# Performance work log

Measured on AMD Instinct MI355X. Metric: run time of the kernel, lower is better.

Reference implementation:

```python
import jax, jax.numpy as jnp
import numpy as np

B, N, IN_DIM, D, H, L = 4, 2048, 1, 256, 8, 4
DH = D // H          # 32 head dim
ROPE_D = DH // 2     # 16 = rotary dim per spatial axis (relative_emb_dim=2)
MIN_FREQ_SCALE = 64.0  # scale / min_freq = 1.0 / (1/64)
EPS = 1e-5


def setup_inputs():
    key = jax.random.key(0)
    ks = jax.random.split(key, 12)
    s = 0.02
    return {
        'h': jax.random.normal(ks[0], (B, N, IN_DIM), jnp.float32),
        'pos': jax.random.uniform(ks[1], (B, N, 2), jnp.float32),
        'proj_w': jax.random.normal(ks[2], (IN_DIM, D), jnp.float32) * s,
        'proj_b': jnp.zeros((D,), jnp.float32),
        'qkv_w': jax.random.normal(ks[3], (L, D, 3 * D), jnp.float32) * s,
        'out_w': jax.random.normal(ks[4], (L, D, D), jnp.float32) * s,
        'out_b': jnp.zeros((L, D), jnp.float32),
        'O_w': jax.random.normal(ks[5], (L, D, D), jnp.float32) * s,
        'O_b': jnp.zeros((L, D), jnp.float32),
        'ffn1_w': jax.random.normal(ks[6], (L, D, 2 * D), jnp.float32) * s,
        'ffn1_b': jnp.zeros((L, 2 * D), jnp.float32),
        'ffn2_w': jax.random.normal(ks[7], (L, 2 * D, D), jnp.float32) * s,
        'ffn2_b': jnp.zeros((L, D), jnp.float32),
        'ln1_g': jnp.ones((L, D), jnp.float32),
        'ln1_b': jnp.zeros((L, D), jnp.float32),
        'ln2_g': jnp.ones((L, D), jnp.float32),
        'ln2_b': jnp.zeros((L, D), jnp.float32),
        'final_w': jax.random.normal(ks[8], (D, D), jnp.float32) * s,
    }


def _rope_freqs(coords):
    # coords: (B, N) -> freqs (B, N, ROPE_D)
    inv_freq = 1.0 / (10000.0 ** (jnp.arange(0, ROPE_D, 2, dtype=jnp.float32) / ROPE_D))
    f = (coords * MIN_FREQ_SCALE)[..., None] * inv_freq
    return jnp.concatenate([f, f], axis=-1)


def _rotate_half(x):
    d = x.shape[-1] // 2
    return jnp.concatenate([-x[..., d:], x[..., :d]], axis=-1)


def _apply_rope(t, f):
    return t * jnp.cos(f) + _rotate_half(t) * jnp.sin(f)


def _apply_2d_rope(t, ft, fx):
    d = t.shape[-1] // 2
    return jnp.concatenate([_apply_rope(t[..., :d], ft), _apply_rope(t[..., d:], fx)], axis=-1)


def _ln(x, g, b):
    m = jnp.mean(x, -1, keepdims=True)
    v = jnp.mean((x - m) ** 2, -1, keepdims=True)
    return (x - m) / jnp.sqrt(v + EPS) * g + b


def _forward(h, pos, proj_w, proj_b, qkv_w, out_w, out_b, O_w, O_b,
             ffn1_w, ffn1_b, ffn2_w, ffn2_b, ln1_g, ln1_b, ln2_g, ln2_b, final_w):
    h = h @ proj_w + proj_b                      # (B, N, D)
    ft = _rope_freqs(pos[..., 0])[:, None]       # (B, 1, N, ROPE_D) broadcast over heads
    fx = _rope_freqs(pos[..., 1])[:, None]
    scale = DH ** -0.5
    for l in range(L):
        qkv = h @ qkv_w[l]                       # (B, N, 3D)
        q, k, v = jnp.split(qkv, 3, axis=-1)
        to_heads = lambda t: t.reshape(B, N, H, DH).transpose(0, 2, 1, 3)
        q, k, v = to_heads(q), to_heads(k), to_heads(v)
        q = _apply_2d_rope(q, ft, fx)
        k = _apply_2d_rope(k, ft, fx)
        attn = jax.nn.softmax(jnp.einsum('bhid,bhjd->bhij', q, k) * scale, axis=-1)
        o = jnp.einsum('bhij,bhjd->bhid', attn, v)
        o = o.transpose(0, 2, 1, 3).reshape(B, N, D)
        o = o @ out_w[l] + out_b[l]              # attention to_out
        o = o @ O_w[l] + O_b[l]                  # layer O projection
        h = _ln(h + o, ln1_g[l], ln1_b[l])
        f = jax.nn.relu(h @ ffn1_w[l] + ffn1_b[l]) @ ffn2_w[l] + ffn2_b[l]
        h = _ln(h + f, ln2_g[l], ln2_b[l])
    return h @ final_w


def reference(h, pos, proj_w, proj_b, qkv_w, out_w, out_b, O_w, O_b,
              ffn1_w, ffn1_b, ffn2_w, ffn2_b, ln1_g, ln1_b, ln2_g, ln2_b, final_w):
    return _forward(h, pos, proj_w, proj_b, qkv_w, out_w, out_b, O_w, O_b,
                    ffn1_w, ffn1_b, ffn2_w, ffn2_b, ln1_g, ln1_b, ln2_g, ln2_b, final_w)
```

## Files before the change

### kernel.cpp

```cpp
#include <hip/hip_runtime.h>
#include <math.h>

#define B_ 4
#define N_ 2048
#define D_ 256
#define H_ 8
#define L_ 4
#define DH_ 32

typedef float f32x4 __attribute__((ext_vector_type(4)));
typedef short short8 __attribute__((ext_vector_type(8)));
typedef unsigned short ushort_t;
typedef ushort_t ushortx4 __attribute__((ext_vector_type(4)));
typedef ushort_t ushortx8 __attribute__((ext_vector_type(8)));

static __device__ __forceinline__ ushort_t f2bf(float x) {
    unsigned int u = __float_as_uint(x);
    unsigned int r = (u + 0x7fffu + ((u >> 16) & 1u)) >> 16;
    return (ushort_t)r;
}

static __device__ __forceinline__ unsigned int cvt_pk_bf16(float a, float b) {
    unsigned int w;
    asm("v_cvt_pk_bf16_f32 %0, %1, %2" : "=v"(w) : "v"(a), "v"(b));
    return w;
}

__global__ __launch_bounds__(256) void proj_kernel(
    const float* __restrict__ hin, const float* __restrict__ w,
    const float* __restrict__ bias, float* __restrict__ hout,
    ushort_t* __restrict__ hb)
{
    long idx = (long)blockIdx.x * 256 + threadIdx.x;
    long bn = idx >> 6;
    int d4 = (int)(idx & 63) << 2;
    float hv = hin[bn];
    float4 wv = *(const float4*)&w[d4];
    float4 bv = *(const float4*)&bias[d4];
    float4 o;
    o.x = hv * wv.x + bv.x;
    o.y = hv * wv.y + bv.y;
    o.z = hv * wv.z + bv.z;
    o.w = hv * wv.w + bv.w;
    *(float4*)&hout[bn * D_ + d4] = o;
    ushortx4 ob;
    ob[0] = f2bf(o.x); ob[1] = f2bf(o.y); ob[2] = f2bf(o.z); ob[3] = f2bf(o.w);
    *(ushortx4*)&hb[bn * D_ + d4] = ob;
}

__global__ __launch_bounds__(256) void rope_table_kernel(
    const float* __restrict__ pos, float* __restrict__ tab)
{
    int i = blockIdx.x * 256 + threadIdx.x;
    if (i >= B_ * N_) return;
    float t = pos[i * 2 + 0] * 64.0f;
    float x = pos[i * 2 + 1] * 64.0f;
    float* o = tab + (long)i * 32;
    const float log2_1e4_over8 = 13.28771237954945f / 8.0f;
    #pragma unroll
    for (int j = 0; j < 8; ++j) {
        float invf = exp2f(-(float)j * log2_1e4_over8);
        float st, ct, sx, cx;
        sincosf(t * invf, &st, &ct);
        sincosf(x * invf, &sx, &cx);
        o[j]      = ct;
        o[8 + j]  = st;
        o[16 + j] = cx;
        o[24 + j] = sx;
    }
}

__global__ __launch_bounds__(256) void rope_convert_kernel(
    const float* __restrict__ qkv, const float* __restrict__ tab,
    ushort_t* __restrict__ Qb, ushort_t* __restrict__ Kb)
{
    const float F = 0.17677669529663687f * 1.4426950408889634f;
    long idx = (long)blockIdx.x * 256 + threadIdx.x;
    int p = (int)(idx & 15);
    int h = (int)((idx >> 4) & 7);
    long bn = idx >> 7;
    int half = p >> 3;
    int j = p & 7;
    const float* tb = tab + bn * 32;
    float c = tb[half * 16 + j];
    float s = tb[half * 16 + 8 + j];
    float cF = c * F, sF = s * F;
    int b = (int)(bn >> 11);
    int n = (int)(bn & 2047);
    long obase = ((long)(b * H_ + h) * N_ + n) * DH_;
    const float* base = qkv + bn * (3 * D_) + h * DH_ + half * 16 + j;
    int d0 = half * 16 + j;
    float q0 = base[0], q1 = base[8];
    Qb[obase + d0]     = f2bf(q0 * cF - q1 * sF);
    Qb[obase + d0 + 8] = f2bf(q1 * cF + q0 * sF);
    float k0 = base[D_], k1 = base[D_ + 8];
    Kb[obase + d0]     = f2bf(k0 * c - k1 * s);
    Kb[obase + d0 + 8] = f2bf(k1 * c + k0 * s);
}

__global__ __launch_bounds__(256) void vtrans_kernel(
    const float* __restrict__ qkv, ushort_t* __restrict__ Vt)
{
    int bh = blockIdx.y;
    int b = bh >> 3, h = bh & 7;
    int n0 = blockIdx.x << 6;
    __shared__ float T[64][36];
    int t = threadIdx.x;
    int r = t >> 2, c0 = (t & 3) << 3;
    const float* src = qkv + ((long)b * N_ + n0 + r) * (3 * D_) + 2 * D_ + h * DH_ + c0;
    float4 a = ((const float4*)src)[0];
    float4 bb = ((const float4*)src)[1];
    *(float4*)&T[r][c0] = a;
    *(float4*)&T[r][c0 + 4] = bb;
    __syncthreads();
    int d = t >> 3, n8 = (t & 7) << 3;
    ushortx8 o;
    #pragma unroll
    for (int i = 0; i < 8; ++i) o[i] = f2bf(T[n8 + i][d]);
    *(ushortx8*)&Vt[((long)bh * DH_ + d) * N_ + n0 + n8] = o;
}

__global__ __launch_bounds__(256) void wprep_kernel(
    const float* __restrict__ qkv_w, const float* __restrict__ out_w,
    const float* __restrict__ O_w, const float* __restrict__ ffn1_w,
    const float* __restrict__ ffn2_w, const float* __restrict__ final_w,
    ushort_t* __restrict__ WT)
{
    int bid = blockIdx.x;
    const float* src; ushort_t* dst; int K, Nn, tile;
    if (bid < 192)      { int l = bid / 48;        tile = bid % 48;        src = qkv_w  + (long)l * 196608; dst = WT + (long)l * 196608;           K = 256; Nn = 768; }
    else if (bid < 256) { int r = bid - 192; int l = r / 16; tile = r % 16; src = out_w  + (long)l * 65536;  dst = WT + 786432  + (long)l * 65536;  K = 256; Nn = 256; }
    else if (bid < 320) { int r = bid - 256; int l = r / 16; tile = r % 16; src = O_w    + (long)l * 65536;  dst = WT + 1048576 + (long)l * 65536;  K = 256; Nn = 256; }
    else if (bid < 448) { int r = bid - 320; int l = r / 32; tile = r % 32; src = ffn1_w + (long)l * 131072; dst = WT + 1310720 + (long)l * 131072; K = 256; Nn = 512; }
    else if (bid < 576) { int r = bid - 448; int l = r / 32; tile = r % 32; src = ffn2_w + (long)l * 131072; dst = WT + 1835008 + (long)l * 131072; K = 512; Nn = 256; }
    else                { tile = bid - 576;                                 src = final_w;                   dst = WT + 2359296;                    K = 256; Nn = 256; }
    int ntn = Nn >> 6;
    int kt = (tile / ntn) << 6;
    int nt = (tile % ntn) << 6;
    __shared__ float Tl[64][65];
    int t = threadIdx.x;
    int kr = t >> 2, nc0 = (t & 3) << 4;
    const float* sp = src + (long)(kt + kr) * Nn + nt + nc0;
    float4 v0 = ((const float4*)sp)[0];
    float4 v1 = ((const float4*)sp)[1];
    float4 v2 = ((const float4*)sp)[2];
    float4 v3 = ((const float4*)sp)[3];
    float* tr = &Tl[kr][nc0];
    tr[0] = v0.x; tr[1] = v0.y; tr[2] = v0.z; tr[3] = v0.w;
    tr[4] = v1.x; tr[5] = v1.y; tr[6] = v1.z; tr[7] = v1.w;
    tr[8] = v2.x; tr[9] = v2.y; tr[10] = v2.z; tr[11] = v2.w;
    tr[12] = v3.x; tr[13] = v3.y; tr[14] = v3.z; tr[15] = v3.w;
    __syncthreads();
    int n = t >> 2, kc0 = (t & 3) << 4;
    ushortx8 o0, o1;
    #pragma unroll
    for (int i = 0; i < 8; ++i) o0[i] = f2bf(Tl[kc0 + i][n]);
    #pragma unroll
    for (int i = 0; i < 8; ++i) o1[i] = f2bf(Tl[kc0 + 8 + i][n]);
    ushort_t* dp = dst + (long)(nt + n) * K + kt + kc0;
    *(ushortx8*)dp = o0;
    *(ushortx8*)(dp + 8) = o1;
}

__global__ __launch_bounds__(256) void gemm_mfma(
    const ushort_t* __restrict__ A, const ushort_t* __restrict__ BT,
    const float* __restrict__ bias, void* __restrict__ Cout,
    int N, int K, int flags)
{
    __shared__ ushort_t sA[64 * 64];
    __shared__ ushort_t sB[64 * 64];
    int tid = threadIdx.x;
    int wid = tid >> 6, lane = tid & 63;
    int lo = lane & 15, hi = lane >> 4;
    int wm = wid >> 1, wn = wid & 1;
    int m0 = blockIdx.y << 6, n0 = blockIdx.x << 6;

    int srow = tid >> 3;
    int sslot = tid & 7;
    const ushort_t* Ap  = A  + (long)(m0 + srow) * K + sslot * 8;
    const ushort_t* Ap2 = Ap + 32 * (long)K;
    const ushort_t* Bp  = BT + (long)(n0 + srow) * K + sslot * 8;
    const ushort_t* Bp2 = Bp + 32 * (long)K;
    int wa1 = srow * 64 + (sslot ^ (srow & 7)) * 8;
    int wa2 = (srow + 32) * 64 + (sslot ^ (srow & 7)) * 8;

    f32x4 acc[2][2];
    #pragma unroll
    for (int i = 0; i < 2; ++i)
        #pragma unroll
        for (int j = 0; j < 2; ++j) acc[i][j] = (f32x4){0.f, 0.f, 0.f, 0.f};

    int ar0 = (wm * 32 + lo) * 64;
    int ar1 = (wm * 32 + 16 + lo) * 64;
    int br0 = (wn * 32 + lo) * 64;
    int br1 = (wn * 32 + 16 + lo) * 64;
    int swz = lo & 7;

    for (int kt = 0; kt < K; kt += 64) {
        ushortx8 a1 = *(const ushortx8*)(Ap + kt);
        ushortx8 a2 = *(const ushortx8*)(Ap2 + kt);
        ushortx8 b1 = *(const ushortx8*)(Bp + kt);
        ushortx8 b2 = *(const ushortx8*)(Bp2 + kt);
        __syncthreads();
        *(ushortx8*)&sA[wa1] = a1;
        *(ushortx8*)&sA[wa2] = a2;
        *(ushortx8*)&sB[wa1] = b1;
        *(ushortx8*)&sB[wa2] = b2;
        __syncthreads();
        #pragma unroll
        for (int kf = 0; kf < 2; ++kf) {
            int ks = ((kf * 4 + hi) ^ swz) * 8;
            short8 a0 = *(const short8*)&sA[ar0 + ks];
            short8 a1f = *(const short8*)&sA[ar1 + ks];
            short8 b0 = *(const short8*)&sB[br0 + ks];
            short8 b1f = *(const short8*)&sB[br1 + ks];
            acc[0][0] = __builtin_amdgcn_mfma_f32_16x16x32_bf16(a0, b0, acc[0][0], 0, 0, 0);
            acc[0][1] = __builtin_amdgcn_mfma_f32_16x16x32_bf16(a0, b1f, acc[0][1], 0, 0, 0);
            acc[1][0] = __builtin_amdgcn_mfma_f32_16x16x32_bf16(a1f, b0, acc[1][0], 0, 0, 0);
            acc[1][1] = __builtin_amdgcn_mfma_f32_16x16x32_bf16(a1f, b1f, acc[1][1], 0, 0, 0);
        }
    }

    #pragma unroll
    for (int nf = 0; nf < 2; ++nf) {
        int col = n0 + wn * 32 + nf * 16 + lo;
        float bv = (flags & 1) ? bias[col] : 0.f;
        #pragma unroll
        for (int mf = 0; mf < 2; ++mf) {
            #pragma unroll
            for (int j = 0; j < 4; ++j) {
                float v = acc[mf][nf][j] + bv;
                if (flags & 2) v = fmaxf(v, 0.f);
                long row = m0 + wm * 32 + mf * 16 + hi * 4 + j;
                if (flags & 4) ((ushort_t*)Cout)[row * N + col] = f2bf(v);
                else           ((float*)Cout)[row * N + col] = v;
            }
        }
    }
}

__global__ __launch_bounds__(256) void attn_mfma2(
    const ushort_t* __restrict__ Qb, const ushort_t* __restrict__ Kb,
    const ushort_t* __restrict__ Vt, ushort_t* __restrict__ o)
{
    int bh = blockIdx.y;
    int tid = threadIdx.x;
    int wid = tid >> 6, lane = tid & 63;
    int lo = lane & 15, hi = lane >> 4;
    int q0 = (blockIdx.x << 6) + wid * 16;

    __shared__ ushort_t Vl[2][32][136];
    __shared__ ushort_t Pl[4][16][136];

    const ushort_t* Qbase = Qb + (long)bh * N_ * DH_;
    const ushort_t* Kbase = Kb + (long)bh * N_ * DH_;
    const ushort_t* Vbase = Vt + (long)bh * DH_ * N_;

    short8 qf = *(const short8*)&Qbase[(long)(q0 + lo) * DH_ + hi * 8];

    int vrow = tid >> 4;
    int vc8 = (tid & 15) << 3;

    {
        short8 v0 = *(const short8*)&Vbase[(long)vrow * N_ + vc8];
        short8 v1 = *(const short8*)&Vbase[(long)(vrow + 16) * N_ + vc8];
        *(short8*)&Vl[0][vrow][vc8] = v0;
        *(short8*)&Vl[0][vrow + 16][vc8] = v1;
    }
    __syncthreads();

    float m = -1e30f, l = 0.f;
    f32x4 acc0 = {0.f, 0.f, 0.f, 0.f}, acc1 = {0.f, 0.f, 0.f, 0.f};

    for (int it = 0; it < N_ / 128; ++it) {
        int k0 = it << 7;
        int buf = it & 1;
        short8 nv0, nv1;
        if (it < N_ / 128 - 1) {
            nv0 = *(const short8*)&Vbase[(long)vrow * N_ + k0 + 128 + vc8];
            nv1 = *(const short8*)&Vbase[(long)(vrow + 16) * N_ + k0 + 128 + vc8];
        }
        f32x4 s[8];
        const f32x4 zz = {0.f, 0.f, 0.f, 0.f};
        #pragma unroll
        for (int t = 0; t < 8; ++t) {
            short8 kf = *(const short8*)&Kbase[(long)(k0 + 16 * t + lo) * DH_ + hi * 8];
            s[t] = __builtin_amdgcn_mfma_f32_16x16x32_bf16(kf, qf, zz, 0, 0, 0);
        }
        f32x4 m4 = s[0];
        #pragma unroll
        for (int t = 1; t < 8; ++t) {
            m4[0] = fmaxf(m4[0], s[t][0]); m4[1] = fmaxf(m4[1], s[t][1]);
            m4[2] = fmaxf(m4[2], s[t][2]); m4[3] = fmaxf(m4[3], s[t][3]);
        }
        float pmax = fmaxf(fmaxf(m4[0], m4[1]), fmaxf(m4[2], m4[3]));
        pmax = fmaxf(pmax, __shfl_xor(pmax, 16, 64));
        pmax = fmaxf(pmax, __shfl_xor(pmax, 32, 64));
        if (!__all(pmax <= m + 8.f)) {
            float mn = fmaxf(m, pmax);
            float corr = __builtin_amdgcn_exp2f(m - mn);
            m = mn;
            l *= corr;
            acc0 *= corr;
            acc1 *= corr;
        }
        #pragma unroll
        for (int t = 0; t < 8; ++t) {
            s[t][0] = __builtin_amdgcn_exp2f(s[t][0] - m);
            s[t][1] = __builtin_amdgcn_exp2f(s[t][1] - m);
            s[t][2] = __builtin_amdgcn_exp2f(s[t][2] - m);
            s[t][3] = __builtin_amdgcn_exp2f(s[t][3] - m);
        }
        f32x4 sv = s[0];
        #pragma unroll
        for (int t = 1; t < 8; ++t) sv += s[t];
        float sum = (sv[0] + sv[1]) + (sv[2] + sv[3]);
        sum += __shfl_xor(sum, 16, 64);
        sum += __shfl_xor(sum, 32, 64);
        l += sum;
        {
            unsigned int* Pw = (unsigned int*)&Pl[wid][lo][0];
            #pragma unroll
            for (int t = 0; t < 8; ++t) {
                Pw[8 * t + 2 * hi]     = cvt_pk_bf16(s[t][0], s[t][1]);
                Pw[8 * t + 2 * hi + 1] = cvt_pk_bf16(s[t][2], s[t][3]);
            }
        }
        if (it < N_ / 128 - 1) {
            *(short8*)&Vl[buf ^ 1][vrow][vc8] = nv0;
            *(short8*)&Vl[buf ^ 1][vrow + 16][vc8] = nv1;
        }
        #pragma unroll
        for (int c = 0; c < 4; ++c) {
            short8 pa  = *(const short8*)&Pl[wid][lo][32 * c + 8 * hi];
            short8 vb0 = *(const short8*)&Vl[buf][lo][32 * c + 8 * hi];
            short8 vb1 = *(const short8*)&Vl[buf][16 + lo][32 * c + 8 * hi];
            acc0 = __builtin_amdgcn_mfma_f32_16x16x32_bf16(pa, vb0, acc0, 0, 0, 0);
            acc1 = __builtin_amdgcn_mfma_f32_16x16x32_bf16(pa, vb1, acc1, 0, 0, 0);
        }
        __syncthreads();
    }

    float invl = 1.f / l;
    int b = bh >> 3, h = bh & 7;
    #pragma unroll
    for (int j = 0; j < 4; ++j) {
        float iv = __shfl(invl, 4 * hi + j, 64);
        long row = (long)b * N_ + q0 + 4 * hi + j;
        o[row * D_ + h * DH_ + lo]      = f2bf(acc0[j] * iv);
        o[row * D_ + h * DH_ + 16 + lo] = f2bf(acc1[j] * iv);
    }
}

__global__ __launch_bounds__(256) void add_ln_kernel(
    float* __restrict__ h, const float* __restrict__ r,
    const float* __restrict__ g, const float* __restrict__ be,
    ushort_t* __restrict__ hb)
{
    int row = blockIdx.x * 4 + (threadIdx.x >> 6);
    int lane = threadIdx.x & 63;
    long off = (long)row * D_ + (lane << 2);
    float4 x = *(float4*)&h[off];
    float4 rr = *(const float4*)&r[off];
    x.x += rr.x; x.y += rr.y; x.z += rr.z; x.w += rr.w;
    float s = x.x + x.y + x.z + x.w;
    #pragma unroll
    for (int k = 1; k < 64; k <<= 1) s += __shfl_xor(s, k, 64);
    float mean = s * (1.f / 256.f);
    float dx = x.x - mean, dy = x.y - mean, dz = x.z - mean, dw = x.w - mean;
    float sq = dx * dx + dy * dy + dz * dz + dw * dw;
    #pragma unroll
    for (int k = 1; k < 64; k <<= 1) sq += __shfl_xor(sq, k, 64);
    float rstd = rsqrtf(sq * (1.f / 256.f) + 1e-5f);
    float4 gv = *(const float4*)&g[lane << 2];
    float4 bv = *(const float4*)&be[lane << 2];
    float4 o;
    o.x = dx * rstd * gv.x + bv.x;
    o.y = dy * rstd * gv.y + bv.y;
    o.z = dz * rstd * gv.z + bv.z;
    o.w = dw * rstd * gv.w + bv.w;
    *(float4*)&h[off] = o;
    ushortx4 ob;
    ob[0] = f2bf(o.x); ob[1] = f2bf(o.y); ob[2] = f2bf(o.z); ob[3] = f2bf(o.w);
    *(ushortx4*)&hb[off] = ob;
}

extern "C" void kernel_launch(void* const* d_in, const int* in_sizes, int n_in,
                              void* d_out, int out_size, void* d_ws, size_t ws_size,
                              hipStream_t stream) {
    const float* h_in    = (const float*)d_in[0];
    const float* pos     = (const float*)d_in[1];
    const float* proj_w  = (const float*)d_in[2];
    const float* proj_b  = (const float*)d_in[3];
    const float* qkv_w   = (const float*)d_in[4];
    const float* out_w   = (const float*)d_in[5];
    const float* out_b   = (const float*)d_in[6];
    const float* O_w     = (const float*)d_in[7];
    const float* O_b     = (const float*)d_in[8];
    const float* ffn1_w  = (const float*)d_in[9];
    const float* ffn1_b  = (const float*)d_in[10];
    const float* ffn2_w  = (const float*)d_in[11];
    const float* ffn2_b  = (const float*)d_in[12];
    const float* ln1_g   = (const float*)d_in[13];
    const float* ln1_b   = (const float*)d_in[14];
    const float* ln2_g   = (const float*)d_in[15];
    const float* ln2_b   = (const float*)d_in[16];
    const float* final_w = (const float*)d_in[17];
    float* out = (float*)d_out;

    float* ws   = (float*)d_ws;
    float* h    = ws;
    float* hb_f = h + 2097152;
    float* tab  = hb_f + 1048576;
    float* WT_f = tab + 262144;
    float* R    = WT_f + 1212416;
    float* QKV  = R + 6291456;
    float* tf   = QKV + 3145728;

    ushort_t* hb  = (ushort_t*)hb_f;
    ushort_t* WT  = (ushort_t*)WT_f;
    float*    qkvf = R;
    ushort_t* aob = (ushort_t*)R;
    ushort_t* t1b = (ushort_t*)(R + 1048576);
    ushort_t* fb  = (ushort_t*)(R + 2097152);
    ushort_t* Qb  = (ushort_t*)QKV;
    ushort_t* Kb  = Qb + 2097152;
    ushort_t* Vtg = Kb + 2097152;

    const long qkvT_off  = 0;
    const long outT_off  = 786432;
    const long OT_off    = 1048576;
    const long ffn1T_off = 1310720;
    const long ffn2T_off = 1835008;
    const long finT_off  = 2359296;

    const long M = (long)B_ * N_;

    wprep_kernel<<<592, 256, 0, stream>>>(qkv_w, out_w, O_w, ffn1_w, ffn2_w, final_w, WT);
    proj_kernel<<<(M * 64) / 256, 256, 0, stream>>>(h_in, proj_w, proj_b, h, hb);
    rope_table_kernel<<<(B_ * N_) / 256, 256, 0, stream>>>(pos, tab);

    for (int l = 0; l < L_; ++l) {
        gemm_mfma<<<dim3(768 / 64, M / 64), 256, 0, stream>>>(
            hb, WT + qkvT_off + (long)l * 196608, nullptr, qkvf, 768, 256, 0);
        rope_convert_kernel<<<(M * H_ * 16) / 256, 256, 0, stream>>>(qkvf, tab, Qb, Kb);
        vtrans_kernel<<<dim3(N_ / 64, B_ * H_), 256, 0, stream>>>(qkvf, Vtg);
        attn_mfma2<<<dim3(N_ / 64, B_ * H_), 256, 0, stream>>>(Qb, Kb, Vtg, aob);
        gemm_mfma<<<dim3(256 / 64, M / 64), 256, 0, stream>>>(
            aob, WT + outT_off + (long)l * 65536, out_b + (long)l * D_, t1b, 256, 256, 1 | 4);
        gemm_mfma<<<dim3(256 / 64, M / 64), 256, 0, stream>>>(
            t1b, WT + OT_off + (long)l * 65536, O_b + (long)l * D_, tf, 256, 256, 1);
        add_ln_kernel<<<M / 4, 256, 0, stream>>>(
            h, tf, ln1_g + (long)l * D_, ln1_b + (long)l * D_, hb);
        gemm_mfma<<<dim3(512 / 64, M / 64), 256, 0, stream>>>(
            hb, WT + ffn1T_off + (long)l * 131072, ffn1_b + (long)l * 2 * D_, fb, 512, 256, 1 | 2 | 4);
        gemm_mfma<<<dim3(256 / 64, M / 64), 256, 0, stream>>>(
            fb, WT + ffn2T_off + (long)l * 131072, ffn2_b + (long)l * D_, tf, 256, 512, 1);
        add_ln_kernel<<<M / 4, 256, 0, stream>>>(
            h, tf, ln2_g + (long)l * D_, ln2_b + (long)l * D_, hb);
    }
    gemm_mfma<<<dim3(256 / 64, M / 64), 256, 0, stream>>>(
        hb, WT + finT_off, nullptr, out, 256, 256, 0);
}
```

Before: 565.3 us.

## Fold out/O projections, fuse GEMM with residual LayerNorm, rewrite attention with 32x32 MFMA

Three independent changes. First, the out_w and O_w weights (and their biases) are precomputed into a single folded matrix per layer, which removes one GEMM per layer. Second, the two post-GEMM add+LayerNorm kernels become a fused gemm_ln kernel that computes a 16-row by 256-column tile, adds the residual and normalizes it in registers. Third, attention is rewritten to use 32x32x16 MFMA, passing P in registers via permlane32 swaps instead of LDS staging and reading V directly from global memory. The folded product changes rounding, the single-pass variance is less stable, and the fused GEMM has no LDS reuse and launches few large tiles.

```diff
diff --git a/kernel.cpp b/kernel.cpp
--- a/kernel.cpp
+++ b/kernel.cpp
@@ -9,6 +9,7 @@
 #define DH_ 32
 
 typedef float f32x4 __attribute__((ext_vector_type(4)));
+typedef float f32x16 __attribute__((ext_vector_type(16)));
 typedef short short8 __attribute__((ext_vector_type(8)));
 typedef unsigned short ushort_t;
 typedef ushort_t ushortx4 __attribute__((ext_vector_type(4)));
@@ -162,6 +163,68 @@
     *(ushortx8*)(dp + 8) = o1;
 }
 
+__global__ __launch_bounds__(256) void wfold_kernel(
+    const float* __restrict__ out_w, const float* __restrict__ O_w,
+    ushort_t* __restrict__ WTp)
+{
+    int l = blockIdx.x >> 4;
+    int t4 = blockIdx.x & 15;
+    int k0 = (t4 >> 2) << 6, n0 = (t4 & 3) << 6;
+    const float* Am = out_w + (long)l * 65536;
+    const float* Bm = O_w + (long)l * 65536;
+    ushort_t* dst = WTp + (long)l * 65536;
+    __shared__ float sA[16][68];
+    __shared__ float sB[16][64];
+    int tid = threadIdx.x;
+    int tx = tid & 15, ty = tid >> 4;
+    int arow = tid >> 2, acol = (tid & 3) << 2;
+    int brow = tid >> 4, bcol = (tid & 15) << 2;
+    const float* Aptr = Am + (long)(k0 + arow) * 256 + acol;
+    const float* Bptr = Bm + (long)brow * 256 + n0 + bcol;
+    float acc[4][4] = {{0.f}};
+    for (int jt = 0; jt < 256; jt += 16) {
+        float4 av = *(const float4*)(Aptr + jt);
+        float4 bv = *(const float4*)(Bptr + (long)jt * 256);
+        __syncthreads();
+        sA[acol + 0][arow] = av.x;
+        sA[acol + 1][arow] = av.y;
+        sA[acol + 2][arow] = av.z;
+        sA[acol + 3][arow] = av.w;
+        *(float4*)&sB[brow][bcol] = bv;
+        __syncthreads();
+        #pragma unroll
+        for (int kk = 0; kk < 16; ++kk) {
+            float4 a = *(const float4*)&sA[kk][ty << 2];
+            float4 b = *(const float4*)&sB[kk][tx << 2];
+            acc[0][0] += a.x * b.x; acc[0][1] += a.x * b.y; acc[0][2] += a.x * b.z; acc[0][3] += a.x * b.w;
+            acc[1][0] += a.y * b.x; acc[1][1] += a.y * b.y; acc[1][2] += a.y * b.z; acc[1][3] += a.y * b.w;
+            acc[2][0] += a.z * b.x; acc[2][1] += a.z * b.y; acc[2][2] += a.z * b.z; acc[2][3] += a.z * b.w;
+            acc[3][0] += a.w * b.x; acc[3][1] += a.w * b.y; acc[3][2] += a.w * b.z; acc[3][3] += a.w * b.w;
+        }
+    }
+    #pragma unroll
+    for (int i = 0; i < 4; ++i) {
+        int k = k0 + (ty << 2) + i;
+        #pragma unroll
+        for (int c = 0; c < 4; ++c) {
+            int n = n0 + (tx << 2) + c;
+            dst[(long)n * 256 + k] = f2bf(acc[i][c]);
+        }
+    }
+}
+
+__global__ __launch_bounds__(256) void bfold_kernel(
+    const float* __restrict__ out_b, const float* __restrict__ O_w,
+    const float* __restrict__ O_b, float* __restrict__ bp)
+{
+    int l = blockIdx.x;
+    int n = threadIdx.x;
+    const float* Bm = O_w + (long)l * 65536;
+    float acc = O_b[l * 256 + n];
+    for (int j = 0; j < 256; ++j) acc += out_b[l * 256 + j] * Bm[(long)j * 256 + n];
+    bp[l * 256 + n] = acc;
+}
+
 __global__ __launch_bounds__(256) void gemm_mfma(
     const ushort_t* __restrict__ A, const ushort_t* __restrict__ BT,
     const float* __restrict__ bias, void* __restrict__ Cout,
@@ -239,150 +302,174 @@
     }
 }
 
-__global__ __launch_bounds__(256) void attn_mfma2(
+template<int K>
+__global__ __launch_bounds__(256) void gemm_ln(
+    const ushort_t* __restrict__ A, const ushort_t* __restrict__ BT,
+    const float* __restrict__ bias, float* __restrict__ h,
+    ushort_t* __restrict__ hb,
+    const float* __restrict__ g, const float* __restrict__ be)
+{
+    __shared__ float red[4][2][16];
+    int tid = threadIdx.x;
+    int wid = tid >> 6, lane = tid & 63;
+    int lo = lane & 15, hi = lane >> 4;
+    int m0 = blockIdx.x << 4;
+
+    f32x4 acc[4];
+    #pragma unroll
+    for (int f = 0; f < 4; ++f) acc[f] = (f32x4){0.f, 0.f, 0.f, 0.f};
+
+    const ushort_t* Ap = A + (long)(m0 + lo) * K + hi * 8;
+    int colb = (wid << 6) + lo;
+    #pragma unroll
+    for (int kk = 0; kk < K; kk += 32) {
+        short8 af = *(const short8*)(Ap + kk);
+        #pragma unroll
+        for (int f = 0; f < 4; ++f) {
+            short8 bf = *(const short8*)&BT[(long)(colb + (f << 4)) * K + kk + hi * 8];
+            acc[f] = __builtin_amdgcn_mfma_f32_16x16x32_bf16(af, bf, acc[f], 0, 0, 0);
+        }
+    }
+
+    float vv[4][4];
+    float rs[4] = {0.f, 0.f, 0.f, 0.f}, rq[4] = {0.f, 0.f, 0.f, 0.f};
+    #pragma unroll
+    for (int f = 0; f < 4; ++f) {
+        int col = colb + (f << 4);
+        float bv = bias[col];
+        #pragma unroll
+        for (int j = 0; j < 4; ++j) {
+            int row = m0 + hi * 4 + j;
+            float v = acc[f][j] + bv + h[(long)row * D_ + col];
+            vv[f][j] = v;
+            rs[j] += v;
+            rq[j] += v * v;
+        }
+    }
+    #pragma unroll
+    for (int j = 0; j < 4; ++j) {
+        #pragma unroll
+        for (int k = 1; k < 16; k <<= 1) {
+            rs[j] += __shfl_xor(rs[j], k, 64);
+            rq[j] += __shfl_xor(rq[j], k, 64);
+        }
+    }
+    if (lo == 0) {
+        #pragma unroll
+        for (int j = 0; j < 4; ++j) {
+            red[wid][0][hi * 4 + j] = rs[j];
+            red[wid][1][hi * 4 + j] = rq[j];
+        }
+    }
+    __syncthreads();
+    float mean[4], rstd[4];
+    #pragma unroll
+    for (int j = 0; j < 4; ++j) {
+        int row = hi * 4 + j;
+        float s = red[0][0][row] + red[1][0][row] + red[2][0][row] + red[3][0][row];
+        float q = red[0][1][row] + red[1][1][row] + red[2][1][row] + red[3][1][row];
+        mean[j] = s * (1.f / 256.f);
+        float var = q * (1.f / 256.f) - mean[j] * mean[j];
+        rstd[j] = rsqrtf(var + 1e-5f);
+    }
+    #pragma unroll
+    for (int f = 0; f < 4; ++f) {
+        int col = colb + (f << 4);
+        float gv = g[col], bev = be[col];
+        #pragma unroll
+        for (int j = 0; j < 4; ++j) {
+            long row = m0 + hi * 4 + j;
+            float o = (vv[f][j] - mean[j]) * rstd[j] * gv + bev;
+            h[row * D_ + col] = o;
+            hb[row * D_ + col] = f2bf(o);
+        }
+    }
+}
+
+__global__ __launch_bounds__(256) void attn_mfma3(
     const ushort_t* __restrict__ Qb, const ushort_t* __restrict__ Kb,
     const ushort_t* __restrict__ Vt, ushort_t* __restrict__ o)
 {
     int bh = blockIdx.y;
     int tid = threadIdx.x;
     int wid = tid >> 6, lane = tid & 63;
-    int lo = lane & 15, hi = lane >> 4;
-    int q0 = (blockIdx.x << 6) + wid * 16;
-
-    __shared__ ushort_t Vl[2][32][136];
-    __shared__ ushort_t Pl[4][16][136];
-
-    const ushort_t* Qbase = Qb + (long)bh * N_ * DH_;
-    const ushort_t* Kbase = Kb + (long)bh * N_ * DH_;
-    const ushort_t* Vbase = Vt + (long)bh * DH_ * N_;
-
-    short8 qf = *(const short8*)&Qbase[(long)(q0 + lo) * DH_ + hi * 8];
-
-    int vrow = tid >> 4;
-    int vc8 = (tid & 15) << 3;
-
-    {
-        short8 v0 = *(const short8*)&Vbase[(long)vrow * N_ + vc8];
-        short8 v1 = *(const short8*)&Vbase[(long)(vrow + 16) * N_ + vc8];
-        *(short8*)&Vl[0][vrow][vc8] = v0;
-        *(short8*)&Vl[0][vrow + 16][vc8] = v1;
-    }
-    __syncthreads();
-
-    float m = -1e30f, l = 0.f;
-    f32x4 acc0 = {0.f, 0.f, 0.f, 0.f}, acc1 = {0.f, 0.f, 0.f, 0.f};
-
-    for (int it = 0; it < N_ / 128; ++it) {
-        int k0 = it << 7;
-        int buf = it & 1;
-        short8 nv0, nv1;
-        if (it < N_ / 128 - 1) {
-            nv0 = *(const short8*)&Vbase[(long)vrow * N_ + k0 + 128 + vc8];
-            nv1 = *(const short8*)&Vbase[(long)(vrow + 16) * N_ + k0 + 128 + vc8];
-        }
-        f32x4 s[8];
-        const f32x4 zz = {0.f, 0.f, 0.f, 0.f};
-        #pragma unroll
-        for (int t = 0; t < 8; ++t) {
-            short8 kf = *(const short8*)&Kbase[(long)(k0 + 16 * t + lo) * DH_ + hi * 8];
-            s[t] = __builtin_amdgcn_mfma_f32_16x16x32_bf16(kf, qf, zz, 0, 0, 0);
-        }
-        f32x4 m4 = s[0];
-        #pragma unroll
-        for (int t = 1; t < 8; ++t) {
-            m4[0] = fmaxf(m4[0], s[t][0]); m4[1] = fmaxf(m4[1], s[t][1]);
-            m4[2] = fmaxf(m4[2], s[t][2]); m4[3] = fmaxf(m4[3], s[t][3]);
-        }
-        float pmax = fmaxf(fmaxf(m4[0], m4[1]), fmaxf(m4[2], m4[3]));
-        pmax = fmaxf(pmax, __shfl_xor(pmax, 16, 64));
+    int lq = lane & 31;
+    int half = lane >> 5;
+    int qbase = (blockIdx.x << 7) + wid * 32;
+
+    const ushort_t* Qp = Qb + (long)bh * N_ * DH_;
+    const ushort_t* Kp = Kb + (long)bh * N_ * DH_;
+    const ushort_t* Vp = Vt + (long)bh * DH_ * N_;
+
+    short8 qf0 = *(const short8*)&Qp[(long)(qbase + lq) * DH_ + half * 8];
+    short8 qf1 = *(const short8*)&Qp[(long)(qbase + lq) * DH_ + 16 + half * 8];
+
+    f32x16 acc;
+    #pragma unroll
+    for (int r = 0; r < 16; ++r) acc[r] = 0.f;
+    float m = -1e30f, lsum = 0.f;
+
+    for (int k0 = 0; k0 < N_; k0 += 32) {
+        short8 kf0 = *(const short8*)&Kp[(long)(k0 + lq) * DH_ + half * 8];
+        short8 kf1 = *(const short8*)&Kp[(long)(k0 + lq) * DH_ + 16 + half * 8];
+        f32x16 s;
+        #pragma unroll
+        for (int r = 0; r < 16; ++r) s[r] = 0.f;
+        s = __builtin_amdgcn_mfma_f32_32x32x16_bf16(kf0, qf0, s, 0, 0, 0);
+        s = __builtin_amdgcn_mfma_f32_32x32x16_bf16(kf1, qf1, s, 0, 0, 0);
+
+        float pmax = s[0];
+        #pragma unroll
+        for (int r = 1; r < 16; ++r) pmax = fmaxf(pmax, s[r]);
         pmax = fmaxf(pmax, __shfl_xor(pmax, 32, 64));
+
         if (!__all(pmax <= m + 8.f)) {
             float mn = fmaxf(m, pmax);
             float corr = __builtin_amdgcn_exp2f(m - mn);
             m = mn;
-            l *= corr;
-            acc0 *= corr;
-            acc1 *= corr;
-        }
-        #pragma unroll
-        for (int t = 0; t < 8; ++t) {
-            s[t][0] = __builtin_amdgcn_exp2f(s[t][0] - m);
-            s[t][1] = __builtin_amdgcn_exp2f(s[t][1] - m);
-            s[t][2] = __builtin_amdgcn_exp2f(s[t][2] - m);
-            s[t][3] = __builtin_amdgcn_exp2f(s[t][3] - m);
-        }
-        f32x4 sv = s[0];
-        #pragma unroll
-        for (int t = 1; t < 8; ++t) sv += s[t];
-        float sum = (sv[0] + sv[1]) + (sv[2] + sv[3]);
-        sum += __shfl_xor(sum, 16, 64);
+            lsum *= corr;
+            #pragma unroll
+            for (int r = 0; r < 16; ++r) {
+                int qr = (r & 3) + 8 * (r >> 2) + 4 * half;
+                acc[r] *= __shfl(corr, qr, 64);
+            }
+        }
+        float sum = 0.f;
+        #pragma unroll
+        for (int r = 0; r < 16; ++r) {
+            s[r] = __builtin_amdgcn_exp2f(s[r] - m);
+            sum += s[r];
+        }
         sum += __shfl_xor(sum, 32, 64);
-        l += sum;
-        {
-            unsigned int* Pw = (unsigned int*)&Pl[wid][lo][0];
-            #pragma unroll
-            for (int t = 0; t < 8; ++t) {
-                Pw[8 * t + 2 * hi]     = cvt_pk_bf16(s[t][0], s[t][1]);
-                Pw[8 * t + 2 * hi + 1] = cvt_pk_bf16(s[t][2], s[t][3]);
-            }
-        }
-        if (it < N_ / 128 - 1) {
-            *(short8*)&Vl[buf ^ 1][vrow][vc8] = nv0;
-            *(short8*)&Vl[buf ^ 1][vrow + 16][vc8] = nv1;
-        }
-        #pragma unroll
-        for (int c = 0; c < 4; ++c) {
-            short8 pa  = *(const short8*)&Pl[wid][lo][32 * c + 8 * hi];
-            short8 vb0 = *(const short8*)&Vl[buf][lo][32 * c + 8 * hi];
-            short8 vb1 = *(const short8*)&Vl[buf][16 + lo][32 * c + 8 * hi];
-            acc0 = __builtin_amdgcn_mfma_f32_16x16x32_bf16(pa, vb0, acc0, 0, 0, 0);
-            acc1 = __builtin_amdgcn_mfma_f32_16x16x32_bf16(pa, vb1, acc1, 0, 0, 0);
-        }
-        __syncthreads();
-    }
-
-    float invl = 1.f / l;
+        lsum += sum;
+
+        unsigned int w0 = cvt_pk_bf16(s[0], s[1]),   w1 = cvt_pk_bf16(s[2], s[3]);
+        unsigned int w2 = cvt_pk_bf16(s[4], s[5]),   w3 = cvt_pk_bf16(s[6], s[7]);
+        unsigned int w4 = cvt_pk_bf16(s[8], s[9]),   w5 = cvt_pk_bf16(s[10], s[11]);
+        unsigned int w6 = cvt_pk_bf16(s[12], s[13]), w7 = cvt_pk_bf16(s[14], s[15]);
+        asm volatile("v_permlane32_swap_b32 %0, %1" : "+v"(w0), "+v"(w2));
+        asm volatile("v_permlane32_swap_b32 %0, %1" : "+v"(w1), "+v"(w3));
+        asm volatile("v_permlane32_swap_b32 %0, %1" : "+v"(w4), "+v"(w6));
+        asm volatile("v_permlane32_swap_b32 %0, %1" : "+v"(w5), "+v"(w7));
+        union { unsigned int u[4]; short8 s8; } pa0, pa1;
+        pa0.u[0] = w0; pa0.u[1] = w1; pa0.u[2] = w2; pa0.u[3] = w3;
+        pa1.u[0] = w4; pa1.u[1] = w5; pa1.u[2] = w6; pa1.u[3] = w7;
+
+        short8 vb0 = *(const short8*)&Vp[(long)lq * N_ + k0 + half * 8];
+        short8 vb1 = *(const short8*)&Vp[(long)lq * N_ + k0 + 16 + half * 8];
+        acc = __builtin_amdgcn_mfma_f32_32x32x16_bf16(pa0.s8, vb0, acc, 0, 0, 0);
+        acc = __builtin_amdgcn_mfma_f32_32x32x16_bf16(pa1.s8, vb1, acc, 0, 0, 0);
+    }
+
+    float invl = 1.f / lsum;
     int b = bh >> 3, h = bh & 7;
     #pragma unroll
-    for (int j = 0; j < 4; ++j) {
-        float iv = __shfl(invl, 4 * hi + j, 64);
-        long row = (long)b * N_ + q0 + 4 * hi + j;
-        o[row * D_ + h * DH_ + lo]      = f2bf(acc0[j] * iv);
-        o[row * D_ + h * DH_ + 16 + lo] = f2bf(acc1[j] * iv);
-    }
-}
-
-__global__ __launch_bounds__(256) void add_ln_kernel(
-    float* __restrict__ h, const float* __restrict__ r,
-    const float* __restrict__ g, const float* __restrict__ be,
-    ushort_t* __restrict__ hb)
-{
-    int row = blockIdx.x * 4 + (threadIdx.x >> 6);
-    int lane = threadIdx.x & 63;
-    long off = (long)row * D_ + (lane << 2);
-    float4 x = *(float4*)&h[off];
-    float4 rr = *(const float4*)&r[off];
-    x.x += rr.x; x.y += rr.y; x.z += rr.z; x.w += rr.w;
-    float s = x.x + x.y + x.z + x.w;
-    #pragma unroll
-    for (int k = 1; k < 64; k <<= 1) s += __shfl_xor(s, k, 64);
-    float mean = s * (1.f / 256.f);
-    float dx = x.x - mean, dy = x.y - mean, dz = x.z - mean, dw = x.w - mean;
-    float sq = dx * dx + dy * dy + dz * dz + dw * dw;
-    #pragma unroll
-    for (int k = 1; k < 64; k <<= 1) sq += __shfl_xor(sq, k, 64);
-    float rstd = rsqrtf(sq * (1.f / 256.f) + 1e-5f);
-    float4 gv = *(const float4*)&g[lane << 2];
-    float4 bv = *(const float4*)&be[lane << 2];
-    float4 o;
-    o.x = dx * rstd * gv.x + bv.x;
-    o.y = dy * rstd * gv.y + bv.y;
-    o.z = dz * rstd * gv.z + bv.z;
-    o.w = dw * rstd * gv.w + bv.w;
-    *(float4*)&h[off] = o;
-    ushortx4 ob;
-    ob[0] = f2bf(o.x); ob[1] = f2bf(o.y); ob[2] = f2bf(o.z); ob[3] = f2bf(o.w);
-    *(ushortx4*)&hb[off] = ob;
+    for (int r = 0; r < 16; ++r) {
+        int qr = (r & 3) + 8 * (r >> 2) + 4 * half;
+        float iv = __shfl(invl, qr, 64);
+        long row = (long)b * N_ + qbase + qr;
+        o[row * D_ + h * DH_ + lq] = f2bf(acc[r] * iv);
+    }
 }
 
 extern "C" void kernel_launch(void* const* d_in, const int* in_sizes, int n_in,
@@ -421,15 +508,14 @@
     ushort_t* WT  = (ushort_t*)WT_f;
     float*    qkvf = R;
     ushort_t* aob = (ushort_t*)R;
-    ushort_t* t1b = (ushort_t*)(R + 1048576);
     ushort_t* fb  = (ushort_t*)(R + 2097152);
     ushort_t* Qb  = (ushort_t*)QKV;
     ushort_t* Kb  = Qb + 2097152;
     ushort_t* Vtg = Kb + 2097152;
+    ushort_t* WTp = (ushort_t*)tf;
+    float*    bp  = tf + 131072;
 
     const long qkvT_off  = 0;
-    const long outT_off  = 786432;
-    const long OT_off    = 1048576;
     const long ffn1T_off = 1310720;
     const long ffn2T_off = 1835008;
     const long finT_off  = 2359296;
@@ -437,6 +523,8 @@
     const long M = (long)B_ * N_;
 
     wprep_kernel<<<592, 256, 0, stream>>>(qkv_w, out_w, O_w, ffn1_w, ffn2_w, final_w, WT);
+    wfold_kernel<<<64, 256, 0, stream>>>(out_w, O_w, WTp);
+    bfold_kernel<<<4, 256, 0, stream>>>(out_b, O_w, O_b, bp);
     proj_kernel<<<(M * 64) / 256, 256, 0, stream>>>(h_in, proj_w, proj_b, h, hb);
     rope_table_kernel<<<(B_ * N_) / 256, 256, 0, stream>>>(pos, tab);
 
@@ -445,19 +533,15 @@
             hb, WT + qkvT_off + (long)l * 196608, nullptr, qkvf, 768, 256, 0);
         rope_convert_kernel<<<(M * H_ * 16) / 256, 256, 0, stream>>>(qkvf, tab, Qb, Kb);
         vtrans_kernel<<<dim3(N_ / 64, B_ * H_), 256, 0, stream>>>(qkvf, Vtg);
-        attn_mfma2<<<dim3(N_ / 64, B_ * H_), 256, 0, stream>>>(Qb, Kb, Vtg, aob);
-        gemm_mfma<<<dim3(256 / 64, M / 64), 256, 0, stream>>>(
-            aob, WT + outT_off + (long)l * 65536, out_b + (long)l * D_, t1b, 256, 256, 1 | 4);
-        gemm_mfma<<<dim3(256 / 64, M / 64), 256, 0, stream>>>(
-            t1b, WT + OT_off + (long)l * 65536, O_b + (long)l * D_, tf, 256, 256, 1);
-        add_ln_kernel<<<M / 4, 256, 0, stream>>>(
-            h, tf, ln1_g + (long)l * D_, ln1_b + (long)l * D_, hb);
+        attn_mfma3<<<dim3(N_ / 128, B_ * H_), 256, 0, stream>>>(Qb, Kb, Vtg, aob);
+        gemm_ln<256><<<M / 16, 256, 0, stream>>>(
+            aob, WTp + (long)l * 65536, bp + (long)l * 256, h, hb,
+            ln1_g + (long)l * D_, ln1_b + (long)l * D_);
         gemm_mfma<<<dim3(512 / 64, M / 64), 256, 0, stream>>>(
             hb, WT + ffn1T_off + (long)l * 131072, ffn1_b + (long)l * 2 * D_, fb, 512, 256, 1 | 2 | 4);
-        gemm_mfma<<<dim3(256 / 64, M / 64), 256, 0, stream>>>(
-            fb, WT + ffn2T_off + (long)l * 131072, ffn2_b + (long)l * D_, tf, 256, 512, 1);
-        add_ln_kernel<<<M / 4, 256, 0, stream>>>(
-            h, tf, ln2_g + (long)l * D_, ln2_b + (long)l * D_, hb);
+        gemm_ln<512><<<M / 16, 256, 0, stream>>>(
+            fb, WT + ffn2T_off + (long)l * 131072, ffn2_b + (long)l * D_, h, hb,
+            ln2_g + (long)l * D_, ln2_b + (long)l * D_);
     }
     gemm_mfma<<<dim3(256 / 64, M / 64), 256, 0, stream>>>(
         hb, WT + finT_off, nullptr, out, 256, 256, 0);
```

Result: slower. 633.8 us (+12.1%).
